# Kernel optimization log

Hardware: AMD Instinct MI355X
Metric: run time of the kernel (lower is better)

The kernel has to match this reference:

```python
import jax, jax.numpy as jnp
import numpy as np

D_MODEL = 1024
N_HEADS = 16
HEAD_DIM = D_MODEL // N_HEADS
B, L = 2, 2048


def setup_inputs() -> dict:
    key = jax.random.key(0)
    ks = jax.random.split(key, 12)
    s = 1.0 / np.sqrt(D_MODEL)
    inp = {
        'q': jax.random.normal(ks[0], (B, L, D_MODEL), dtype=jnp.float32),
        'k': jax.random.normal(ks[1], (B, L, D_MODEL), dtype=jnp.float32),
        'v': jax.random.normal(ks[2], (B, L, D_MODEL), dtype=jnp.float32),
        'Wq': jax.random.uniform(ks[3], (D_MODEL, D_MODEL), jnp.float32, -s, s),
        'bq': jax.random.uniform(ks[4], (D_MODEL,), jnp.float32, -s, s),
        'Wk': jax.random.uniform(ks[5], (D_MODEL, D_MODEL), jnp.float32, -s, s),
        'bk': jax.random.uniform(ks[6], (D_MODEL,), jnp.float32, -s, s),
        'Wv': jax.random.uniform(ks[7], (D_MODEL, D_MODEL), jnp.float32, -s, s),
        'bv': jax.random.uniform(ks[8], (D_MODEL,), jnp.float32, -s, s),
        'Wo': jax.random.uniform(ks[9], (D_MODEL, D_MODEL), jnp.float32, -s, s),
        'bo': jax.random.uniform(ks[10], (D_MODEL,), jnp.float32, -s, s),
    }
    return inp


def _heads(x):
    # (B, L, D) -> (B, H, L, Dh)
    b, l, _ = x.shape
    return x.reshape(b, l, N_HEADS, HEAD_DIM).transpose(0, 2, 1, 3)


def reference(q, k, v, Wq, bq, Wk, bk, Wv, bv, Wo, bo):
    # Linear projections (torch Linear: x @ W.T + b)
    qh = _heads(q @ Wq.T + bq)
    kh = _heads(k @ Wk.T + bk)
    vh = _heads(v @ Wv.T + bv)
    scale = 1.0 / jnp.sqrt(jnp.asarray(HEAD_DIM, dtype=qh.dtype))
    scores = jnp.einsum('bhqd,bhkd->bhqk', qh, kh) * scale  # (B,H,L,L)
    attn = jax.nn.softmax(scores, axis=-1)
    out = jnp.einsum('bhqk,bhkd->bhqd', attn, vh)
    out = out.transpose(0, 2, 1, 3).reshape(q.shape[0], q.shape[1], D_MODEL)
    return out @ Wo.T + bo
```

## Files before the change

### kernel.cpp

```cpp
#include <hip/hip_runtime.h>

typedef unsigned short u16;
typedef __bf16 bf16x8 __attribute__((ext_vector_type(8)));
typedef float f32x4 __attribute__((ext_vector_type(4)));
typedef float f32x16 __attribute__((ext_vector_type(16)));
typedef unsigned short u16x8 __attribute__((ext_vector_type(8)));
typedef unsigned int u32x2 __attribute__((ext_vector_type(2)));
typedef unsigned int u32x4 __attribute__((ext_vector_type(4)));

#define LSEQ 2048
#define DM 1024
#define NH 16
#define HD 64
#define SCALE_Q 0.1803368801111244f

__device__ __forceinline__ u16 f2bf(float f) {
  union { float f; unsigned int u; } x;
  x.f = f;
  unsigned int u = x.u;
  u += 0x7FFFu + ((u >> 16) & 1u);
  return (u16)(u >> 16);
}

__device__ __forceinline__ float fexp2(float x) {
  return __builtin_amdgcn_exp2f(x);
}

__device__ __forceinline__ void async16(const void* g, void* l) {
  __builtin_amdgcn_global_load_lds(
      (const __attribute__((address_space(1))) void*)g,
      (__attribute__((address_space(3))) void*)l, 16, 0, 0);
}

__device__ __forceinline__ f32x4 mfma16(bf16x8 a, bf16x8 b, f32x4 c) {
  return __builtin_amdgcn_mfma_f32_16x16x32_bf16(a, b, c, 0, 0, 0);
}
__device__ __forceinline__ f32x16 mfma32(bf16x8 a, bf16x8 b, f32x16 c) {
  return __builtin_amdgcn_mfma_f32_32x32x16_bf16(a, b, c, 0, 0, 0);
}

__device__ __forceinline__ unsigned cvtpk(float lo, float hi) {
  unsigned r;
  asm("v_cvt_pk_bf16_f32 %0, %1, %2" : "=v"(r) : "v"(lo), "v"(hi));
  return r;
}
__device__ __forceinline__ void pswap(unsigned &a, unsigned &b) {
  asm("v_permlane32_swap_b32 %0, %1" : "+v"(a), "+v"(b));
}
__device__ __forceinline__ bf16x8 mk8(unsigned w0, unsigned w1, unsigned w2, unsigned w3) {
  union { unsigned u[4]; bf16x8 v; } x;
  x.u[0] = w0; x.u[1] = w1; x.u[2] = w2; x.u[3] = w3;
  return x.v;
}
__device__ __forceinline__ f32x16 zero16() {
  f32x16 z;
#pragma unroll
  for (int i = 0; i < 16; ++i) z[i] = 0.f;
  return z;
}

__global__ __launch_bounds__(256) void cvt7(
    const float* __restrict__ a0, const float* __restrict__ a1,
    const float* __restrict__ a2, const float* __restrict__ a3,
    const float* __restrict__ a4, const float* __restrict__ a5,
    const float* __restrict__ a6,
    u16* __restrict__ b0, u16* __restrict__ b1, u16* __restrict__ b2,
    u16* __restrict__ b3, u16* __restrict__ b4, u16* __restrict__ b5,
    u16* __restrict__ b6)
{
  const int t = blockIdx.y;
  const float* s; u16* d; int n;
  switch (t) {
    case 0: s = a0; d = b0; n = 1 << 22; break;
    case 1: s = a1; d = b1; n = 1 << 22; break;
    case 2: s = a2; d = b2; n = 1 << 22; break;
    case 3: s = a3; d = b3; n = 1 << 20; break;
    case 4: s = a4; d = b4; n = 1 << 20; break;
    case 5: s = a5; d = b5; n = 1 << 20; break;
    default: s = a6; d = b6; n = 1 << 20; break;
  }
  const int i = (blockIdx.x * 256 + threadIdx.x) * 8;
  if (i >= n) return;
  f32x4 f0 = *(const f32x4*)(s + i);
  f32x4 f1 = *(const f32x4*)(s + i + 4);
  u16x8 h;
#pragma unroll
  for (int j = 0; j < 4; ++j) { h[j] = f2bf(f0[j]); h[4 + j] = f2bf(f1[j]); }
  *(u16x8*)(d + i) = h;
}

__global__ __launch_bounds__(256) void gemm_qkv(
    const u16* __restrict__ Xq, const u16* __restrict__ Xk, const u16* __restrict__ Xv,
    const u16* __restrict__ Wqb, const u16* __restrict__ Wkb, const u16* __restrict__ Wvb,
    const float* __restrict__ bq, const float* __restrict__ bk, const float* __restrict__ bv,
    u16* __restrict__ Qp, u16* __restrict__ Kp, u16* __restrict__ Vt)
{
  __shared__ __align__(16) u16 As[2][128 * 32];
  __shared__ __align__(16) u16 Bs[2][128 * 32];

  const int tid = threadIdx.x;
  const int lane = tid & 63;
  const int wid = tid >> 6;
  const int lr = lane & 15, lg = lane >> 4;
  const int wr = wid >> 1, wc = wid & 1;
  const int bm = blockIdx.x;
  const int by = blockIdx.y;
  const int wsel = by >> 3;
  const int bn = by & 7;

  const u16* A    = (wsel == 0) ? Xq  : (wsel == 1) ? Xk  : Xv;
  const u16* Bt   = (wsel == 0) ? Wqb : (wsel == 1) ? Wkb : Wvb;
  const float* bias = (wsel == 0) ? bq : (wsel == 1) ? bk : bv;

  const int r0 = tid >> 2;
  const int c0 = (tid & 3) * 8;
  const size_t arow0 = (size_t)(bm * 128 + r0) * DM;
  const size_t arow1 = (size_t)(bm * 128 + 64 + r0) * DM;
  const size_t brow0 = (size_t)(bn * 128 + r0) * DM;
  const size_t brow1 = (size_t)(bn * 128 + 64 + r0) * DM;

  f32x4 acc[4][4];
#pragma unroll
  for (int m = 0; m < 4; ++m)
#pragma unroll
    for (int n = 0; n < 4; ++n) {
      f32x4 z = {0.f, 0.f, 0.f, 0.f};
      acc[m][n] = z;
    }

  async16(A + arow0 + c0, &As[0][tid * 8]);
  async16(A + arow1 + c0, &As[0][2048 + tid * 8]);
  async16(Bt + brow0 + c0, &Bs[0][tid * 8]);
  async16(Bt + brow1 + c0, &Bs[0][2048 + tid * 8]);
  __syncthreads();

  for (int kt = 0; kt < 32; ++kt) {
    const int cur = kt & 1, nxt = cur ^ 1;
    if (kt + 1 < 32) {
      const int kk = (kt + 1) * 32;
      async16(A + arow0 + kk + c0, &As[nxt][tid * 8]);
      async16(A + arow1 + kk + c0, &As[nxt][2048 + tid * 8]);
      async16(Bt + brow0 + kk + c0, &Bs[nxt][tid * 8]);
      async16(Bt + brow1 + kk + c0, &Bs[nxt][2048 + tid * 8]);
    }
    bf16x8 af[4], bfr[4];
#pragma unroll
    for (int m = 0; m < 4; ++m)
      af[m] = *(const bf16x8*)&As[cur][(wr * 64 + m * 16 + lr) * 32 + lg * 8];
#pragma unroll
    for (int n = 0; n < 4; ++n)
      bfr[n] = *(const bf16x8*)&Bs[cur][(wc * 64 + n * 16 + lr) * 32 + lg * 8];
#pragma unroll
    for (int m = 0; m < 4; ++m)
#pragma unroll
      for (int n = 0; n < 4; ++n)
        acc[m][n] = mfma16(af[m], bfr[n], acc[m][n]);
    __syncthreads();
  }

  if (wsel < 2) {
    u16* Out = (wsel == 0) ? Qp : Kp;
    const float oscale = (wsel == 0) ? SCALE_Q : 1.0f;
#pragma unroll
    for (int m = 0; m < 4; ++m) {
#pragma unroll
      for (int n = 0; n < 4; ++n) {
        const int col = bn * 128 + wc * 64 + n * 16 + lr;
        const float bv_ = bias[col];
        const int h = col >> 6, d = col & 63;
#pragma unroll
        for (int r = 0; r < 4; ++r) {
          const int row = bm * 128 + wr * 64 + m * 16 + lg * 4 + r;
          const int b = row >> 11, l = row & 2047;
          Out[((size_t)(b * NH + h) * LSEQ + l) * HD + d] =
              f2bf((acc[m][n][r] + bv_) * oscale);
        }
      }
    }
  } else {
    const int row0b = bm * 128 + wr * 64 + lg * 4;
    const int b = (bm * 128) >> 11;
#pragma unroll
    for (int m = 0; m < 4; ++m) {
      const int l0 = (row0b + m * 16) & 2047;
#pragma unroll
      for (int n = 0; n < 4; ++n) {
        const int col = bn * 128 + wc * 64 + n * 16 + lr;
        const float bv_ = bias[col];
        const int h = col >> 6, d = col & 63;
        u32x2 w;
        w[0] = cvtpk(acc[m][n][0] + bv_, acc[m][n][1] + bv_);
        w[1] = cvtpk(acc[m][n][2] + bv_, acc[m][n][3] + bv_);
        *(u32x2*)&Vt[((size_t)(b * NH + h) * HD + d) * LSEQ + l0] = w;
      }
    }
  }
}

__global__ __launch_bounds__(256) void attn_fwd(
    const u16* __restrict__ Qp, const u16* __restrict__ Kp, const u16* __restrict__ Vt,
    u16* __restrict__ ctx)
{
  __shared__ __align__(16) u16 Ks[2][64 * 64];
  __shared__ __align__(16) u16 Vts[2][64 * 64];

  const int tid = threadIdx.x;
  const int wid = tid >> 6;
  const int lane = tid & 63;
  const int lq = lane & 31;
  const int h = lane >> 5;
  const int qt = blockIdx.x, bh = blockIdx.y;

  const u16* Qb = Qp + (size_t)bh * (LSEQ * HD);
  const u16* Kb = Kp + (size_t)bh * (LSEQ * HD);
  const u16* Vb = Vt + (size_t)bh * (HD * LSEQ);

  const int q0 = qt * 128 + wid * 32;

  bf16x8 qf[4];
#pragma unroll
  for (int dk = 0; dk < 4; ++dk)
    qf[dk] = *(const bf16x8*)(Qb + (size_t)(q0 + lq) * HD + dk * 16 + h * 8);

  float l_run = 0.f;
  f32x16 o0 = zero16(), o1 = zero16();

  const int srow = tid >> 3;
  const int sslot = tid & 7;
  const int sswz = (sslot ^ (srow & 7)) << 3;
  const int ksrc = srow * 64 + sswz;
  const size_t vsrc0 = (size_t)srow * LSEQ + sswz;
  const size_t vsrc1 = (size_t)(srow + 32) * LSEQ + sswz;

  {
    async16(Kb + ksrc, &Ks[0][tid * 8]);
    async16(Kb + 2048 + ksrc, &Ks[0][2048 + tid * 8]);
    async16(Vb + vsrc0, &Vts[0][tid * 8]);
    async16(Vb + vsrc1, &Vts[0][2048 + tid * 8]);
  }
  __syncthreads();

  for (int kt = 0; kt < LSEQ / 64; ++kt) {
    const int cur = kt & 1, nxt = cur ^ 1;
    const bool hn = (kt + 1) < LSEQ / 64;
    if (hn) {
      async16(Kb + (kt + 1) * 4096 + ksrc, &Ks[nxt][tid * 8]);
      async16(Kb + (kt + 1) * 4096 + 2048 + ksrc, &Ks[nxt][2048 + tid * 8]);
      async16(Vb + (kt + 1) * 64 + vsrc0, &Vts[nxt][tid * 8]);
      async16(Vb + (kt + 1) * 64 + vsrc1, &Vts[nxt][2048 + tid * 8]);
    }

    f32x16 st0 = zero16(), st1 = zero16();
    __builtin_amdgcn_s_setprio(1);
#pragma unroll
    for (int dk = 0; dk < 4; ++dk) {
      const int g = ((2 * dk + h) ^ (lq & 7)) << 3;
      bf16x8 kf0 = *(const bf16x8*)&Ks[cur][lq * 64 + g];
      bf16x8 kf1 = *(const bf16x8*)&Ks[cur][(32 + lq) * 64 + g];
      st0 = mfma32(kf0, qf[dk], st0);
      st1 = mfma32(kf1, qf[dk], st1);
    }
    __builtin_amdgcn_s_setprio(0);

    float rs = 0.f;
#pragma unroll
    for (int i = 0; i < 16; ++i) { st0[i] = fexp2(st0[i]); rs += st0[i]; }
#pragma unroll
    for (int i = 0; i < 16; ++i) { st1[i] = fexp2(st1[i]); rs += st1[i]; }
    l_run += rs;

    unsigned w[16];
#pragma unroll
    for (int m = 0; m < 4; ++m) {
      w[m * 2 + 0] = cvtpk(st0[4 * m + 0], st0[4 * m + 1]);
      w[m * 2 + 1] = cvtpk(st0[4 * m + 2], st0[4 * m + 3]);
      w[8 + m * 2 + 0] = cvtpk(st1[4 * m + 0], st1[4 * m + 1]);
      w[8 + m * 2 + 1] = cvtpk(st1[4 * m + 2], st1[4 * m + 3]);
    }
#pragma unroll
    for (int n = 0; n < 2; ++n) {
      pswap(w[n * 8 + 0], w[n * 8 + 2]);
      pswap(w[n * 8 + 1], w[n * 8 + 3]);
      pswap(w[n * 8 + 4], w[n * 8 + 6]);
      pswap(w[n * 8 + 5], w[n * 8 + 7]);
    }
    bf16x8 pa[4];
    pa[0] = mk8(w[0], w[1], w[2], w[3]);
    pa[1] = mk8(w[4], w[5], w[6], w[7]);
    pa[2] = mk8(w[8], w[9], w[10], w[11]);
    pa[3] = mk8(w[12], w[13], w[14], w[15]);

    __builtin_amdgcn_s_setprio(1);
#pragma unroll
    for (int ks = 0; ks < 4; ++ks) {
      const int g0g = ((2 * ks + h) ^ (lq & 7)) << 3;
      bf16x8 vf0 = *(const bf16x8*)&Vts[cur][lq * 64 + g0g];
      bf16x8 vf1 = *(const bf16x8*)&Vts[cur][(32 + lq) * 64 + g0g];
      o0 = mfma32(pa[ks], vf0, o0);
      o1 = mfma32(pa[ks], vf1, o1);
    }
    __builtin_amdgcn_s_setprio(0);

    __syncthreads();
  }

  const int b = bh >> 4, head = bh & 15;
  const float ltot = l_run + __shfl_xor(l_run, 32);
  const float linv = 1.0f / ltot;
#pragma unroll
  for (int reg = 0; reg < 16; ++reg) {
    const int row = (reg & 3) + 8 * (reg >> 2) + 4 * h;
    const float iv = __shfl(linv, row);
    const size_t base = ((size_t)(b * LSEQ + q0 + row)) * DM + head * HD;
    ctx[base + lq] = f2bf(o0[reg] * iv);
    ctx[base + 32 + lq] = f2bf(o1[reg] * iv);
  }
}

__global__ __launch_bounds__(256) void gemm_out(
    const u16* __restrict__ Actx, const u16* __restrict__ Wob,
    const float* __restrict__ bo, float* __restrict__ out)
{
  __shared__ __align__(16) u16 As[2][128 * 32];
  __shared__ __align__(16) u16 Bs[2][128 * 32];

  const int tid = threadIdx.x;
  const int lane = tid & 63;
  const int wid = tid >> 6;
  const int lr = lane & 15, lg = lane >> 4;
  const int wr = wid >> 1, wc = wid & 1;
  const int bm = blockIdx.x;
  const int bn = blockIdx.y;

  const int r0 = tid >> 2;
  const int c0 = (tid & 3) * 8;
  const size_t arow0 = (size_t)(bm * 128 + r0) * DM;
  const size_t arow1 = (size_t)(bm * 128 + 64 + r0) * DM;
  const size_t brow0 = (size_t)(bn * 128 + r0) * DM;
  const size_t brow1 = (size_t)(bn * 128 + 64 + r0) * DM;

  f32x4 acc[4][4];
#pragma unroll
  for (int m = 0; m < 4; ++m)
#pragma unroll
    for (int n = 0; n < 4; ++n) {
      f32x4 z = {0.f, 0.f, 0.f, 0.f};
      acc[m][n] = z;
    }

  async16(Actx + arow0 + c0, &As[0][tid * 8]);
  async16(Actx + arow1 + c0, &As[0][2048 + tid * 8]);
  async16(Wob + brow0 + c0, &Bs[0][tid * 8]);
  async16(Wob + brow1 + c0, &Bs[0][2048 + tid * 8]);
  __syncthreads();

  for (int kt = 0; kt < 32; ++kt) {
    const int cur = kt & 1, nxt = cur ^ 1;
    if (kt + 1 < 32) {
      const int kk = (kt + 1) * 32;
      async16(Actx + arow0 + kk + c0, &As[nxt][tid * 8]);
      async16(Actx + arow1 + kk + c0, &As[nxt][2048 + tid * 8]);
      async16(Wob + brow0 + kk + c0, &Bs[nxt][tid * 8]);
      async16(Wob + brow1 + kk + c0, &Bs[nxt][2048 + tid * 8]);
    }
    bf16x8 af[4], bfr[4];
#pragma unroll
    for (int m = 0; m < 4; ++m)
      af[m] = *(const bf16x8*)&As[cur][(wr * 64 + m * 16 + lr) * 32 + lg * 8];
#pragma unroll
    for (int n = 0; n < 4; ++n)
      bfr[n] = *(const bf16x8*)&Bs[cur][(wc * 64 + n * 16 + lr) * 32 + lg * 8];
#pragma unroll
    for (int m = 0; m < 4; ++m)
#pragma unroll
      for (int n = 0; n < 4; ++n)
        acc[m][n] = mfma16(af[m], bfr[n], acc[m][n]);
    __syncthreads();
  }

#pragma unroll
  for (int m = 0; m < 4; ++m) {
#pragma unroll
    for (int n = 0; n < 4; ++n) {
      const int col = bn * 128 + wc * 64 + n * 16 + lr;
      const float bv_ = bo[col];
#pragma unroll
      for (int r = 0; r < 4; ++r) {
        const int row = bm * 128 + wr * 64 + m * 16 + lg * 4 + r;
        out[(size_t)row * DM + col] = acc[m][n][r] + bv_;
      }
    }
  }
}

extern "C" void kernel_launch(void* const* d_in, const int* in_sizes, int n_in,
                              void* d_out, int out_size, void* d_ws, size_t ws_size,
                              hipStream_t stream) {
  const float* q  = (const float*)d_in[0];
  const float* k  = (const float*)d_in[1];
  const float* v  = (const float*)d_in[2];
  const float* Wq = (const float*)d_in[3];
  const float* bq = (const float*)d_in[4];
  const float* Wk = (const float*)d_in[5];
  const float* bk = (const float*)d_in[6];
  const float* Wv = (const float*)d_in[7];
  const float* bv = (const float*)d_in[8];
  const float* Wo = (const float*)d_in[9];
  const float* bo = (const float*)d_in[10];
  float* out = (float*)d_out;

  u16* ws  = (u16*)d_ws;
  u16* Xqb = ws;
  u16* Xkb = Xqb + (4u << 20);
  u16* Xvb = Xkb + (4u << 20);
  u16* Wqb = Xvb + (4u << 20);
  u16* Wkb = Wqb + (1u << 20);
  u16* Wvb = Wkb + (1u << 20);
  u16* Wob = Wvb + (1u << 20);
  u16* Qp  = Wob + (1u << 20);
  u16* Kp  = Qp + (4u << 20);
  u16* Vt  = Kp + (4u << 20);
  u16* ctx = Xqb;

  cvt7<<<dim3(2048, 7), 256, 0, stream>>>(q, k, v, Wq, Wk, Wv, Wo,
                                          Xqb, Xkb, Xvb, Wqb, Wkb, Wvb, Wob);
  gemm_qkv<<<dim3(32, 24), 256, 0, stream>>>(Xqb, Xkb, Xvb, Wqb, Wkb, Wvb,
                                             bq, bk, bv, Qp, Kp, Vt);
  attn_fwd<<<dim3(16, 32), 256, 0, stream>>>(Qp, Kp, Vt, ctx);
  gemm_out<<<dim3(32, 8), 256, 0, stream>>>(ctx, Wob, bo, out);
}
```

Baseline: 149.8 us.

## Triple-buffer LDS pipelines with explicit vmcnt waits and XCD-aware attention block mapping

Moves all three kernels (QKV GEMM, attention, output GEMM) from double to triple LDS buffering, prefetching two stages ahead. The full __syncthreads is replaced by a partial s_waitcnt vmcnt(4) plus a barrier, so the next tile's loads can stay in flight across iterations. MFMA blocks in the GEMMs get raised wave priority. The attention kernel also remaps block IDs so blocks sharing a head land on the same XCD, improving L2 reuse of K/V. The cost is more LDS per block, which may lower occupancy.

```diff
diff --git a/kernel.cpp b/kernel.cpp
--- a/kernel.cpp
+++ b/kernel.cpp
@@ -6,7 +6,6 @@
 typedef float f32x16 __attribute__((ext_vector_type(16)));
 typedef unsigned short u16x8 __attribute__((ext_vector_type(8)));
 typedef unsigned int u32x2 __attribute__((ext_vector_type(2)));
-typedef unsigned int u32x4 __attribute__((ext_vector_type(4)));
 
 #define LSEQ 2048
 #define DM 1024
@@ -58,6 +57,11 @@
   for (int i = 0; i < 16; ++i) z[i] = 0.f;
   return z;
 }
+
+#define WAITBAR4 do { asm volatile("s_waitcnt vmcnt(4) lgkmcnt(0)" ::: "memory"); \
+                      __builtin_amdgcn_s_barrier(); } while (0)
+#define WAITBAR0 do { asm volatile("s_waitcnt vmcnt(0) lgkmcnt(0)" ::: "memory"); \
+                      __builtin_amdgcn_s_barrier(); } while (0)
 
 __global__ __launch_bounds__(256) void cvt7(
     const float* __restrict__ a0, const float* __restrict__ a1,
@@ -95,8 +99,8 @@
     const float* __restrict__ bq, const float* __restrict__ bk, const float* __restrict__ bv,
     u16* __restrict__ Qp, u16* __restrict__ Kp, u16* __restrict__ Vt)
 {
-  __shared__ __align__(16) u16 As[2][128 * 32];
-  __shared__ __align__(16) u16 Bs[2][128 * 32];
+  __shared__ __align__(16) u16 As[3][128 * 32];
+  __shared__ __align__(16) u16 Bs[3][128 * 32];
 
   const int tid = threadIdx.x;
   const int lane = tid & 63;
@@ -119,6 +123,14 @@
   const size_t brow0 = (size_t)(bn * 128 + r0) * DM;
   const size_t brow1 = (size_t)(bn * 128 + 64 + r0) * DM;
 
+#define GSTAGE(t, buf) do { \
+    const int kk_ = (t) * 32; \
+    async16(A + arow0 + kk_ + c0, &As[buf][tid * 8]); \
+    async16(A + arow1 + kk_ + c0, &As[buf][2048 + tid * 8]); \
+    async16(Bt + brow0 + kk_ + c0, &Bs[buf][tid * 8]); \
+    async16(Bt + brow1 + kk_ + c0, &Bs[buf][2048 + tid * 8]); \
+  } while (0)
+
   f32x4 acc[4][4];
 #pragma unroll
   for (int m = 0; m < 4; ++m)
@@ -128,35 +140,35 @@
       acc[m][n] = z;
     }
 
-  async16(A + arow0 + c0, &As[0][tid * 8]);
-  async16(A + arow1 + c0, &As[0][2048 + tid * 8]);
-  async16(Bt + brow0 + c0, &Bs[0][tid * 8]);
-  async16(Bt + brow1 + c0, &Bs[0][2048 + tid * 8]);
-  __syncthreads();
-
+  GSTAGE(0, 0);
+  GSTAGE(1, 1);
+  asm volatile("s_waitcnt vmcnt(4)" ::: "memory");
+  __builtin_amdgcn_s_barrier();
+
+  int cb = 0;
   for (int kt = 0; kt < 32; ++kt) {
-    const int cur = kt & 1, nxt = cur ^ 1;
-    if (kt + 1 < 32) {
-      const int kk = (kt + 1) * 32;
-      async16(A + arow0 + kk + c0, &As[nxt][tid * 8]);
-      async16(A + arow1 + kk + c0, &As[nxt][2048 + tid * 8]);
-      async16(Bt + brow0 + kk + c0, &Bs[nxt][tid * 8]);
-      async16(Bt + brow1 + kk + c0, &Bs[nxt][2048 + tid * 8]);
-    }
+    int sb = cb + 2; if (sb >= 3) sb -= 3;
+    if (kt + 2 < 32) GSTAGE(kt + 2, sb);
     bf16x8 af[4], bfr[4];
 #pragma unroll
     for (int m = 0; m < 4; ++m)
-      af[m] = *(const bf16x8*)&As[cur][(wr * 64 + m * 16 + lr) * 32 + lg * 8];
+      af[m] = *(const bf16x8*)&As[cb][(wr * 64 + m * 16 + lr) * 32 + lg * 8];
 #pragma unroll
     for (int n = 0; n < 4; ++n)
-      bfr[n] = *(const bf16x8*)&Bs[cur][(wc * 64 + n * 16 + lr) * 32 + lg * 8];
+      bfr[n] = *(const bf16x8*)&Bs[cb][(wc * 64 + n * 16 + lr) * 32 + lg * 8];
+    __builtin_amdgcn_s_setprio(1);
 #pragma unroll
     for (int m = 0; m < 4; ++m)
 #pragma unroll
       for (int n = 0; n < 4; ++n)
         acc[m][n] = mfma16(af[m], bfr[n], acc[m][n]);
-    __syncthreads();
-  }
+    __builtin_amdgcn_s_setprio(0);
+    if (kt < 31) {
+      if (kt + 2 < 32) { WAITBAR4; } else { WAITBAR0; }
+    }
+    cb = (cb + 1 == 3) ? 0 : cb + 1;
+  }
+#undef GSTAGE
 
   if (wsel < 2) {
     u16* Out = (wsel == 0) ? Qp : Kp;
@@ -201,15 +213,19 @@
     const u16* __restrict__ Qp, const u16* __restrict__ Kp, const u16* __restrict__ Vt,
     u16* __restrict__ ctx)
 {
-  __shared__ __align__(16) u16 Ks[2][64 * 64];
-  __shared__ __align__(16) u16 Vts[2][64 * 64];
+  __shared__ __align__(16) u16 Ks[3][64 * 64];
+  __shared__ __align__(16) u16 Vts[3][64 * 64];
 
   const int tid = threadIdx.x;
   const int wid = tid >> 6;
   const int lane = tid & 63;
   const int lq = lane & 31;
   const int h = lane >> 5;
-  const int qt = blockIdx.x, bh = blockIdx.y;
+
+  const int lid = blockIdx.x + (int)gridDim.x * blockIdx.y;
+  const int xcd = lid & 7, slot = lid >> 3;
+  const int bh = xcd * 4 + (slot >> 4);
+  const int qt = slot & 15;
 
   const u16* Qb = Qp + (size_t)bh * (LSEQ * HD);
   const u16* Kb = Kp + (size_t)bh * (LSEQ * HD);
@@ -232,31 +248,30 @@
   const size_t vsrc0 = (size_t)srow * LSEQ + sswz;
   const size_t vsrc1 = (size_t)(srow + 32) * LSEQ + sswz;
 
-  {
-    async16(Kb + ksrc, &Ks[0][tid * 8]);
-    async16(Kb + 2048 + ksrc, &Ks[0][2048 + tid * 8]);
-    async16(Vb + vsrc0, &Vts[0][tid * 8]);
-    async16(Vb + vsrc1, &Vts[0][2048 + tid * 8]);
-  }
-  __syncthreads();
-
+#define ASTAGE(t, buf) do { \
+    async16(Kb + (t) * 4096 + ksrc, &Ks[buf][tid * 8]); \
+    async16(Kb + (t) * 4096 + 2048 + ksrc, &Ks[buf][2048 + tid * 8]); \
+    async16(Vb + (t) * 64 + vsrc0, &Vts[buf][tid * 8]); \
+    async16(Vb + (t) * 64 + vsrc1, &Vts[buf][2048 + tid * 8]); \
+  } while (0)
+
+  ASTAGE(0, 0);
+  ASTAGE(1, 1);
+  asm volatile("s_waitcnt vmcnt(4)" ::: "memory");
+  __builtin_amdgcn_s_barrier();
+
+  int cb = 0;
   for (int kt = 0; kt < LSEQ / 64; ++kt) {
-    const int cur = kt & 1, nxt = cur ^ 1;
-    const bool hn = (kt + 1) < LSEQ / 64;
-    if (hn) {
-      async16(Kb + (kt + 1) * 4096 + ksrc, &Ks[nxt][tid * 8]);
-      async16(Kb + (kt + 1) * 4096 + 2048 + ksrc, &Ks[nxt][2048 + tid * 8]);
-      async16(Vb + (kt + 1) * 64 + vsrc0, &Vts[nxt][tid * 8]);
-      async16(Vb + (kt + 1) * 64 + vsrc1, &Vts[nxt][2048 + tid * 8]);
-    }
+    int sb = cb + 2; if (sb >= 3) sb -= 3;
+    if (kt + 2 < LSEQ / 64) ASTAGE(kt + 2, sb);
 
     f32x16 st0 = zero16(), st1 = zero16();
     __builtin_amdgcn_s_setprio(1);
 #pragma unroll
     for (int dk = 0; dk < 4; ++dk) {
       const int g = ((2 * dk + h) ^ (lq & 7)) << 3;
-      bf16x8 kf0 = *(const bf16x8*)&Ks[cur][lq * 64 + g];
-      bf16x8 kf1 = *(const bf16x8*)&Ks[cur][(32 + lq) * 64 + g];
+      bf16x8 kf0 = *(const bf16x8*)&Ks[cb][lq * 64 + g];
+      bf16x8 kf1 = *(const bf16x8*)&Ks[cb][(32 + lq) * 64 + g];
       st0 = mfma32(kf0, qf[dk], st0);
       st1 = mfma32(kf1, qf[dk], st1);
     }
@@ -294,15 +309,19 @@
 #pragma unroll
     for (int ks = 0; ks < 4; ++ks) {
       const int g0g = ((2 * ks + h) ^ (lq & 7)) << 3;
-      bf16x8 vf0 = *(const bf16x8*)&Vts[cur][lq * 64 + g0g];
-      bf16x8 vf1 = *(const bf16x8*)&Vts[cur][(32 + lq) * 64 + g0g];
+      bf16x8 vf0 = *(const bf16x8*)&Vts[cb][lq * 64 + g0g];
+      bf16x8 vf1 = *(const bf16x8*)&Vts[cb][(32 + lq) * 64 + g0g];
       o0 = mfma32(pa[ks], vf0, o0);
       o1 = mfma32(pa[ks], vf1, o1);
     }
     __builtin_amdgcn_s_setprio(0);
 
-    __syncthreads();
-  }
+    if (kt < LSEQ / 64 - 1) {
+      if (kt + 2 < LSEQ / 64) { WAITBAR4; } else { WAITBAR0; }
+    }
+    cb = (cb + 1 == 3) ? 0 : cb + 1;
+  }
+#undef ASTAGE
 
   const int b = bh >> 4, head = bh & 15;
   const float ltot = l_run + __shfl_xor(l_run, 32);
@@ -321,8 +340,8 @@
     const u16* __restrict__ Actx, const u16* __restrict__ Wob,
     const float* __restrict__ bo, float* __restrict__ out)
 {
-  __shared__ __align__(16) u16 As[2][128 * 32];
-  __shared__ __align__(16) u16 Bs[2][128 * 32];
+  __shared__ __align__(16) u16 As[3][128 * 32];
+  __shared__ __align__(16) u16 Bs[3][128 * 32];
 
   const int tid = threadIdx.x;
   const int lane = tid & 63;
@@ -339,6 +358,14 @@
   const size_t brow0 = (size_t)(bn * 128 + r0) * DM;
   const size_t brow1 = (size_t)(bn * 128 + 64 + r0) * DM;
 
+#define GSTAGE(t, buf) do { \
+    const int kk_ = (t) * 32; \
+    async16(Actx + arow0 + kk_ + c0, &As[buf][tid * 8]); \
+    async16(Actx + arow1 + kk_ + c0, &As[buf][2048 + tid * 8]); \
+    async16(Wob + brow0 + kk_ + c0, &Bs[buf][tid * 8]); \
+    async16(Wob + brow1 + kk_ + c0, &Bs[buf][2048 + tid * 8]); \
+  } while (0)
+
   f32x4 acc[4][4];
 #pragma unroll
   for (int m = 0; m < 4; ++m)
@@ -348,35 +375,35 @@
       acc[m][n] = z;
     }
 
-  async16(Actx + arow0 + c0, &As[0][tid * 8]);
-  async16(Actx + arow1 + c0, &As[0][2048 + tid * 8]);
-  async16(Wob + brow0 + c0, &Bs[0][tid * 8]);
-  async16(Wob + brow1 + c0, &Bs[0][2048 + tid * 8]);
-  __syncthreads();
-
+  GSTAGE(0, 0);
+  GSTAGE(1, 1);
+  asm volatile("s_waitcnt vmcnt(4)" ::: "memory");
+  __builtin_amdgcn_s_barrier();
+
+  int cb = 0;
   for (int kt = 0; kt < 32; ++kt) {
-    const int cur = kt & 1, nxt = cur ^ 1;
-    if (kt + 1 < 32) {
-      const int kk = (kt + 1) * 32;
-      async16(Actx + arow0 + kk + c0, &As[nxt][tid * 8]);
-      async16(Actx + arow1 + kk + c0, &As[nxt][2048 + tid * 8]);
-      async16(Wob + brow0 + kk + c0, &Bs[nxt][tid * 8]);
-      async16(Wob + brow1 + kk + c0, &Bs[nxt][2048 + tid * 8]);
-    }
+    int sb = cb + 2; if (sb >= 3) sb -= 3;
+    if (kt + 2 < 32) GSTAGE(kt + 2, sb);
     bf16x8 af[4], bfr[4];
 #pragma unroll
     for (int m = 0; m < 4; ++m)
-      af[m] = *(const bf16x8*)&As[cur][(wr * 64 + m * 16 + lr) * 32 + lg * 8];
+      af[m] = *(const bf16x8*)&As[cb][(wr * 64 + m * 16 + lr) * 32 + lg * 8];
 #pragma unroll
     for (int n = 0; n < 4; ++n)
-      bfr[n] = *(const bf16x8*)&Bs[cur][(wc * 64 + n * 16 + lr) * 32 + lg * 8];
+      bfr[n] = *(const bf16x8*)&Bs[cb][(wc * 64 + n * 16 + lr) * 32 + lg * 8];
+    __builtin_amdgcn_s_setprio(1);
 #pragma unroll
     for (int m = 0; m < 4; ++m)
 #pragma unroll
       for (int n = 0; n < 4; ++n)
         acc[m][n] = mfma16(af[m], bfr[n], acc[m][n]);
-    __syncthreads();
-  }
+    __builtin_amdgcn_s_setprio(0);
+    if (kt < 31) {
+      if (kt + 2 < 32) { WAITBAR4; } else { WAITBAR0; }
+    }
+    cb = (cb + 1 == 3) ? 0 : cb + 1;
+  }
+#undef GSTAGE
 
 #pragma unroll
   for (int m = 0; m < 4; ++m) {
```

Measured after the change: 146.5 us. -2.2%, faster.
